# Optimization experiments

Measured on AMD Instinct MI355X. Metric: run time of the kernel, lower is better.

## Reference

```python
import jax, jax.numpy as jnp
import numpy as np

B, M, N, E = 64, 100, 6400, 102400   # graphs, nodes/graph, total nodes, edges
H, D, EMB, IMG, NC = 4, 512, 768, 1024, 2
HD = H * D
EPS = 1e-5


def _bn2(x, g, b, m, v):
    # BatchNorm1d eval mode on [B, C]
    return (x - m) / jnp.sqrt(v + EPS) * g + b


def _bn3(x, g, b, m, v):
    # BatchNorm1d eval mode on [B, C, L] -> channel dim is axis 1 (node index)
    return (x - m[None, :, None]) / jnp.sqrt(v + EPS)[None, :, None] * g[None, :, None] + b[None, :, None]


def _gat(feat, src, dst, W, al, ar, bias):
    # DGL GATConv (eval: feat_drop is identity). feat: [N, F_in]
    h = (feat @ W.T).reshape(-1, H, D)                 # [N, H, D]
    el = (h * al[None]).sum(-1)                         # [N, H]
    er = (h * ar[None]).sum(-1)                         # [N, H]
    e = jax.nn.leaky_relu(el[src] + er[dst], negative_slope=0.2)  # [E, H]
    mx = jax.ops.segment_max(e, dst, num_segments=N)
    a = jnp.exp(e - mx[dst])
    s = jax.ops.segment_sum(a, dst, num_segments=N)
    alpha = a / s[dst]                                  # edge softmax over incoming edges
    out = jax.ops.segment_sum(h[src] * alpha[:, :, None], dst, num_segments=N)  # [N, H, D]
    return out + bias.reshape(1, H, D)


def setup_inputs() -> dict:
    key = jax.random.key(0)
    ks = iter(jax.random.split(key, 80))
    n = lambda *s: jax.random.normal(next(ks), s, dtype=jnp.float32)

    def bn(c):
        return (1.0 + 0.1 * n(c), 0.1 * n(c), 0.1 * n(c),
                0.5 + jax.random.uniform(next(ks), (c,), dtype=jnp.float32))

    s = 0.02
    inp = {}
    inp['img_embedding'] = n(B, IMG)
    inp['func_text_embedding'] = n(B, EMB)
    inp['unix_emb'] = n(N, EMB)
    inp['pos_emb'] = jax.random.uniform(next(ks), (N, 4), dtype=jnp.float32)
    inp['src'] = jax.random.randint(next(ks), (E,), 0, N)
    inp['dst'] = jax.random.randint(next(ks), (E,), 0, N)
    inp['gat1_W'] = n(HD, EMB) * s; inp['gat1_al'] = n(H, D) * 0.1; inp['gat1_ar'] = n(H, D) * 0.1; inp['gat1_b'] = jnp.zeros(HD)
    inp['gat2_W'] = n(HD, HD) * s; inp['gat2_al'] = n(H, D) * 0.1; inp['gat2_ar'] = n(H, D) * 0.1; inp['gat2_b'] = jnp.zeros(HD)
    inp['fc_W'] = n(D, HD) * s; inp['fc_b'] = jnp.zeros(D)
    inp['hidden_W'] = n(8, D, D) * s; inp['hidden_b'] = jnp.zeros((8, D))
    inp['bn_text_g'], inp['bn_text_b'], inp['bn_text_m'], inp['bn_text_v'] = bn(EMB)
    inp['fc_text_W'] = n(D, EMB) * s; inp['fc_text_b'] = jnp.zeros(D)
    inp['swin_g'], inp['swin_b'], inp['swin_m'], inp['swin_v'] = bn(IMG)
    inp['swinfc_W'] = n(D, IMG) * s; inp['swinfc_b'] = jnp.zeros(D)
    inp['bngat_g'], inp['bngat_b'], inp['bngat_m'], inp['bngat_v'] = bn(M)
    inp['fc_gat_W'] = n(480, D) * s; inp['fc_gat_b'] = jnp.zeros(480)
    inp['bnbb_g'], inp['bnbb_b'], inp['bnbb_m'], inp['bnbb_v'] = bn(M)
    inp['fc_bbox_W'] = n(32, 4) * s; inp['fc_bbox_b'] = jnp.zeros(32)
    inp['fbn_g'], inp['fbn_b'], inp['fbn_m'], inp['fbn_v'] = bn(3 * D)
    inp['final_W'] = n(NC, 3 * D) * s; inp['final_b'] = jnp.zeros(NC)
    return inp


def reference(img_embedding, func_text_embedding, unix_emb, pos_emb, src, dst,
              gat1_W, gat1_al, gat1_ar, gat1_b, gat2_W, gat2_al, gat2_ar, gat2_b,
              fc_W, fc_b, hidden_W, hidden_b,
              bn_text_g, bn_text_b, bn_text_m, bn_text_v, fc_text_W, fc_text_b,
              swin_g, swin_b, swin_m, swin_v, swinfc_W, swinfc_b,
              bngat_g, bngat_b, bngat_m, bngat_v, fc_gat_W, fc_gat_b,
              bnbb_g, bnbb_b, bnbb_m, bnbb_v, fc_bbox_W, fc_bbox_b,
              fbn_g, fbn_b, fbn_m, fbn_v, final_W, final_b):
    # image branch
    x = jax.nn.elu(_bn2(img_embedding, swin_g, swin_b, swin_m, swin_v) @ swinfc_W.T + swinfc_b)
    # text branch
    ft = jax.nn.elu(_bn2(func_text_embedding, bn_text_g, bn_text_b, bn_text_m, bn_text_v) @ fc_text_W.T + fc_text_b)
    # graph branch: two stacked GATConv layers (dropout is identity in eval)
    h = _gat(unix_emb, src, dst, gat1_W, gat1_al, gat1_ar, gat1_b).reshape(N, HD)
    h = _gat(h, src, dst, gat2_W, gat2_al, gat2_ar, gat2_b).reshape(N, HD)
    h = jax.nn.elu(h @ fc_W.T + fc_b)
    for i in range(8):
        h = jax.nn.elu(h @ hidden_W[i].T + hidden_b[i])
    # unbatch + pad to max_node=100 -> pure reshape (all graphs have exactly M nodes)
    h_i = h.reshape(B, M, D)
    pos_i = pos_emb.reshape(B, M, 4)
    h_i = jax.nn.elu(_bn3(h_i, bngat_g, bngat_b, bngat_m, bngat_v) @ fc_gat_W.T + fc_gat_b)      # [B, M, 480]
    pos_i = jax.nn.elu(_bn3(pos_i, bnbb_g, bnbb_b, bnbb_m, bnbb_v) @ fc_bbox_W.T + fc_bbox_b)    # [B, M, 32]
    h_feature = jnp.concatenate([h_i, pos_i], axis=2).mean(axis=1)                                # [B, 512]
    all_feats = jnp.concatenate([x, h_feature, ft], axis=1)                                       # [B, 1536]
    return _bn2(all_feats, fbn_g, fbn_b, fbn_m, fbn_v) @ final_W.T + final_b
```

## Files before the change

### kernel.cpp

```cpp
#include <hip/hip_runtime.h>
#include <math.h>

#define Bg   64
#define Mg   100
#define Ng   6400
#define Eg   102400
#define Hh   4
#define Dd   512
#define HDd  2048
#define EMBd 768
#define IMGd 1024
#define EPSc 1e-5f

typedef __bf16 bf16x8 __attribute__((ext_vector_type(8)));
typedef float  f32x4  __attribute__((ext_vector_type(4)));

__device__ __forceinline__ float eluf(float x) { return x > 0.f ? x : expm1f(x); }

__device__ __forceinline__ unsigned short f2bf(float x) {
    unsigned int u = __builtin_bit_cast(unsigned int, x);
    u += 0x7FFFu + ((u >> 16) & 1u);
    return (unsigned short)(u >> 16);
}
__device__ __forceinline__ float bf2f(unsigned short s) {
    return __builtin_bit_cast(float, ((unsigned int)s) << 16);
}

__device__ __forceinline__ void gld16(const void* g, void* l) {
    __builtin_amdgcn_global_load_lds(
        (const __attribute__((address_space(1))) void*)g,
        (__attribute__((address_space(3))) void*)l, 16, 0, 0);
}

__global__ __launch_bounds__(256)
void gemm_bf16(const unsigned short* __restrict__ A,
               const unsigned short* __restrict__ W,
               const float* __restrict__ bias, void* __restrict__ C,
               int M, int N, int K, int act, int outbf)
{
    __shared__ __align__(16) unsigned short As[128 * 32];
    __shared__ __align__(16) unsigned short Bs[128 * 32];
    const int tid  = threadIdx.x;
    const int lane = tid & 63, wid = tid >> 6;
    const int bm = blockIdx.y * 128, bn = blockIdx.x * 128;
    const int wm = (wid >> 1) * 64, wn = (wid & 1) * 64;
    const int lrow = lane >> 2;
    const int lcol = (lane & 3) << 3;

    f32x4 acc[4][4] = {};

    const int ra = wid * 32;
    const unsigned short* gA0 = A + (size_t)(bm + ra + lrow) * K + lcol;
    const unsigned short* gA1 = A + (size_t)(bm + ra + 16 + lrow) * K + lcol;
    int rb0 = bn + ra + lrow;       if (rb0 >= N) rb0 = N - 1;
    int rb1 = bn + ra + 16 + lrow;  if (rb1 >= N) rb1 = N - 1;
    const unsigned short* gB0 = W + (size_t)rb0 * K + lcol;
    const unsigned short* gB1 = W + (size_t)rb1 * K + lcol;
    unsigned short* lA0 = &As[(ra)      * 32];
    unsigned short* lA1 = &As[(ra + 16) * 32];
    unsigned short* lB0 = &Bs[(ra)      * 32];
    unsigned short* lB1 = &Bs[(ra + 16) * 32];

    const int frow = lane & 15;
    const int quad = (lane >> 4) << 3;

    for (int k0 = 0; k0 < K; k0 += 32) {
        gld16(gA0 + k0, lA0);
        gld16(gA1 + k0, lA1);
        gld16(gB0 + k0, lB0);
        gld16(gB1 + k0, lB1);
        __syncthreads();
        bf16x8 af[4], bfr[4];
#pragma unroll
        for (int i = 0; i < 4; ++i)
            af[i]  = *(const bf16x8*)&As[(wm + i * 16 + frow) * 32 + quad];
#pragma unroll
        for (int i = 0; i < 4; ++i)
            bfr[i] = *(const bf16x8*)&Bs[(wn + i * 16 + frow) * 32 + quad];
#pragma unroll
        for (int mi = 0; mi < 4; ++mi)
#pragma unroll
            for (int ni = 0; ni < 4; ++ni)
                acc[mi][ni] = __builtin_amdgcn_mfma_f32_16x16x32_bf16(
                    af[mi], bfr[ni], acc[mi][ni], 0, 0, 0);
        __syncthreads();
    }

    const int crow0 = bm + wm + ((lane >> 4) << 2);
    const int ccol0 = bn + wn + (lane & 15);
#pragma unroll
    for (int mi = 0; mi < 4; ++mi) {
#pragma unroll
        for (int ni = 0; ni < 4; ++ni) {
            int col = ccol0 + ni * 16;
            if (col >= N) continue;
            float bv = bias ? bias[col] : 0.f;
#pragma unroll
            for (int r = 0; r < 4; ++r) {
                int row = crow0 + mi * 16 + r;
                float v = acc[mi][ni][r] + bv;
                if (act) v = eluf(v);
                if (outbf) ((unsigned short*)C)[(size_t)row * N + col] = f2bf(v);
                else       ((float*)C)[(size_t)row * N + col] = v;
            }
        }
    }
}

__global__ __launch_bounds__(256)
void gemm_bf16_t64(const unsigned short* __restrict__ A,
                   const unsigned short* __restrict__ W,
                   const float* __restrict__ bias, void* __restrict__ C,
                   int M, int N, int K, int act, int outbf)
{
    __shared__ __align__(16) unsigned short As[64 * 32];
    __shared__ __align__(16) unsigned short Bs[64 * 32];
    const int tid  = threadIdx.x;
    const int lane = tid & 63, wid = tid >> 6;
    const int bm = blockIdx.y * 64, bn = blockIdx.x * 64;
    const int wm = (wid >> 1) * 32, wn = (wid & 1) * 32;
    const int lrow = lane >> 2;
    const int lcol = (lane & 3) << 3;

    f32x4 acc[2][2] = {};

    const int ra = wid * 16;
    const unsigned short* gA = A + (size_t)(bm + ra + lrow) * K + lcol;
    int rb = bn + ra + lrow; if (rb >= N) rb = N - 1;
    const unsigned short* gB = W + (size_t)rb * K + lcol;
    unsigned short* lA = &As[ra * 32];
    unsigned short* lB = &Bs[ra * 32];

    const int frow = lane & 15;
    const int quad = (lane >> 4) << 3;

    for (int k0 = 0; k0 < K; k0 += 32) {
        gld16(gA + k0, lA);
        gld16(gB + k0, lB);
        __syncthreads();
        bf16x8 af0 = *(const bf16x8*)&As[(wm + frow) * 32 + quad];
        bf16x8 af1 = *(const bf16x8*)&As[(wm + 16 + frow) * 32 + quad];
        bf16x8 bf0 = *(const bf16x8*)&Bs[(wn + frow) * 32 + quad];
        bf16x8 bf1 = *(const bf16x8*)&Bs[(wn + 16 + frow) * 32 + quad];
        acc[0][0] = __builtin_amdgcn_mfma_f32_16x16x32_bf16(af0, bf0, acc[0][0], 0, 0, 0);
        acc[0][1] = __builtin_amdgcn_mfma_f32_16x16x32_bf16(af0, bf1, acc[0][1], 0, 0, 0);
        acc[1][0] = __builtin_amdgcn_mfma_f32_16x16x32_bf16(af1, bf0, acc[1][0], 0, 0, 0);
        acc[1][1] = __builtin_amdgcn_mfma_f32_16x16x32_bf16(af1, bf1, acc[1][1], 0, 0, 0);
        __syncthreads();
    }

    const int crow0 = bm + wm + ((lane >> 4) << 2);
    const int ccol0 = bn + wn + (lane & 15);
#pragma unroll
    for (int mi = 0; mi < 2; ++mi) {
#pragma unroll
        for (int ni = 0; ni < 2; ++ni) {
            int col = ccol0 + ni * 16;
            if (col >= N) continue;
            float bv = bias ? bias[col] : 0.f;
#pragma unroll
            for (int r = 0; r < 4; ++r) {
                int row = crow0 + mi * 16 + r;
                float v = acc[mi][ni][r] + bv;
                if (act) v = eluf(v);
                if (outbf) ((unsigned short*)C)[(size_t)row * N + col] = f2bf(v);
                else       ((float*)C)[(size_t)row * N + col] = v;
            }
        }
    }
}

__global__ __launch_bounds__(256)
void gemm_nt(const float* __restrict__ A, const float* __restrict__ W,
             const float* __restrict__ bias, float* __restrict__ C,
             int M, int N, int K, int act)
{
    __shared__ float As[16 * 68];
    __shared__ float Ws[16 * 68];
    const int tid = threadIdx.x;
    const int tx = tid & 15, ty = tid >> 4;
    const int bm = blockIdx.y * 64, bn = blockIdx.x * 64;
    const int lrow = tid >> 2;
    const int lk4  = (tid & 3) << 2;
    const int arow = bm + lrow;
    const int wrow = bn + lrow;
    const float* Aptr = A + (size_t)arow * K + lk4;
    const float* Wptr = W + (size_t)wrow * K + lk4;
    float acc[4][4] = {{0.f,0.f,0.f,0.f},{0.f,0.f,0.f,0.f},{0.f,0.f,0.f,0.f},{0.f,0.f,0.f,0.f}};

    for (int k0 = 0; k0 < K; k0 += 16) {
        float4 av = make_float4(0.f,0.f,0.f,0.f);
        float4 wv = make_float4(0.f,0.f,0.f,0.f);
        if (arow < M) av = *(const float4*)(Aptr + k0);
        if (wrow < N) wv = *(const float4*)(Wptr + k0);
        As[(lk4+0)*68 + lrow] = av.x;
        As[(lk4+1)*68 + lrow] = av.y;
        As[(lk4+2)*68 + lrow] = av.z;
        As[(lk4+3)*68 + lrow] = av.w;
        Ws[(lk4+0)*68 + lrow] = wv.x;
        Ws[(lk4+1)*68 + lrow] = wv.y;
        Ws[(lk4+2)*68 + lrow] = wv.z;
        Ws[(lk4+3)*68 + lrow] = wv.w;
        __syncthreads();
#pragma unroll
        for (int kk = 0; kk < 16; ++kk) {
            float4 a = *(const float4*)&As[kk*68 + (ty<<2)];
            float4 w = *(const float4*)&Ws[kk*68 + (tx<<2)];
            acc[0][0] += a.x*w.x; acc[0][1] += a.x*w.y; acc[0][2] += a.x*w.z; acc[0][3] += a.x*w.w;
            acc[1][0] += a.y*w.x; acc[1][1] += a.y*w.y; acc[1][2] += a.y*w.z; acc[1][3] += a.y*w.w;
            acc[2][0] += a.z*w.x; acc[2][1] += a.z*w.y; acc[2][2] += a.z*w.z; acc[2][3] += a.z*w.w;
            acc[3][0] += a.w*w.x; acc[3][1] += a.w*w.y; acc[3][2] += a.w*w.z; acc[3][3] += a.w*w.w;
        }
        __syncthreads();
    }

#pragma unroll
    for (int i = 0; i < 4; ++i) {
        int row = bm + (ty<<2) + i;
        int col = bn + (tx<<2);
        if (row < M && col < N) {
            float4 v;
            v.x = acc[i][0]; v.y = acc[i][1]; v.z = acc[i][2]; v.w = acc[i][3];
            if (bias) { v.x += bias[col]; v.y += bias[col+1]; v.z += bias[col+2]; v.w += bias[col+3]; }
            if (act == 1) { v.x = eluf(v.x); v.y = eluf(v.y); v.z = eluf(v.z); v.w = eluf(v.w); }
            *(float4*)(C + (size_t)row * N + col) = v;
        }
    }
}

struct CvtPack {
    const float* s[6];
    unsigned short* d[6];
    int n4[6];
};

__global__ void cvt_all(CvtPack p, int total4)
{
    int i = blockIdx.x * 256 + threadIdx.x;
    if (i >= total4) return;
#pragma unroll
    for (int k = 0; k < 6; ++k) {
        if (i < p.n4[k]) {
            float4 v = ((const float4*)p.s[k])[i];
            ushort4 o;
            o.x = f2bf(v.x); o.y = f2bf(v.y); o.z = f2bf(v.z); o.w = f2bf(v.w);
            ((ushort4*)p.d[k])[i] = o;
            return;
        }
        i -= p.n4[k];
    }
}

__global__ void bn_col(const float* __restrict__ x, const float* __restrict__ g,
                       const float* __restrict__ b, const float* __restrict__ m,
                       const float* __restrict__ v, float* __restrict__ y,
                       int rows, int cols)
{
    int i = blockIdx.x * 256 + threadIdx.x;
    if (i >= rows * cols) return;
    int c = i % cols;
    float inv = rsqrtf(v[c] + EPSc);
    y[i] = (x[i] - m[c]) * inv * g[c] + b[c];
}

__global__ void bn_node_b4(const ushort4* __restrict__ x, const float* __restrict__ g,
                           const float* __restrict__ b, const float* __restrict__ m,
                           const float* __restrict__ v, ushort4* __restrict__ y,
                           int total4, int Cdim4)
{
    int i = blockIdx.x * 256 + threadIdx.x;
    if (i >= total4) return;
    int n = i / Cdim4;
    int p = n % Mg;
    float sc = rsqrtf(v[p] + EPSc) * g[p];
    float sh = b[p] - m[p] * sc;
    ushort4 xv = x[i];
    ushort4 o;
    o.x = f2bf(bf2f(xv.x) * sc + sh);
    o.y = f2bf(bf2f(xv.y) * sc + sh);
    o.z = f2bf(bf2f(xv.z) * sc + sh);
    o.w = f2bf(bf2f(xv.w) * sc + sh);
    y[i] = o;
}

__global__ void zero_i32(int* __restrict__ p, int n)
{
    int i = blockIdx.x * 256 + threadIdx.x;
    if (i < n) p[i] = 0;
}

__global__ void count_dst(const int* __restrict__ dst, int* __restrict__ counts, int E)
{
    int i = blockIdx.x * 256 + threadIdx.x;
    if (i < E) atomicAdd(&counts[dst[i]], 1);
}

__global__ __launch_bounds__(1024)
void scan_excl(const int* __restrict__ counts, int* __restrict__ offs,
               int* __restrict__ cursor, int n)
{
    __shared__ int sm[1024];
    __shared__ int carry;
    if (threadIdx.x == 0) carry = 0;
    __syncthreads();
    for (int base = 0; base < n; base += 1024) {
        int i = base + (int)threadIdx.x;
        int v = (i < n) ? counts[i] : 0;
        sm[threadIdx.x] = v;
        __syncthreads();
        for (int o = 1; o < 1024; o <<= 1) {
            int t = (threadIdx.x >= (unsigned)o) ? sm[threadIdx.x - o] : 0;
            __syncthreads();
            sm[threadIdx.x] += t;
            __syncthreads();
        }
        int incl = sm[threadIdx.x];
        int myc = carry;
        if (i < n) {
            int ex = myc + incl - v;
            offs[i] = ex;
            cursor[i] = ex;
        }
        __syncthreads();
        if (threadIdx.x == 1023) carry = myc + sm[1023];
        __syncthreads();
    }
    if (threadIdx.x == 0) offs[n] = carry;
}

__global__ void scatter_edges(const int* __restrict__ dst, int* __restrict__ cursor,
                              int* __restrict__ eid, int E)
{
    int i = blockIdx.x * 256 + threadIdx.x;
    if (i < E) {
        int p = atomicAdd(&cursor[dst[i]], 1);
        eid[p] = i;
    }
}

__global__ __launch_bounds__(256)
void elr_kernel(const unsigned short* __restrict__ Hm, const float* __restrict__ al,
                const float* __restrict__ ar, float* __restrict__ el,
                float* __restrict__ er)
{
    int wid = threadIdx.x >> 6, lane = threadIdx.x & 63;
    int g = (blockIdx.x << 2) + wid;
    int n = g >> 2, h = g & 3;
    const unsigned short* hp = Hm + ((size_t)n << 11) + (h << 9) + (lane << 3);
    const float* alp = al + (h << 9) + (lane << 3);
    const float* arp = ar + (h << 9) + (lane << 3);
    ushort4 x0 = *(const ushort4*)hp;
    ushort4 x1 = *(const ushort4*)(hp + 4);
    float4 l0 = *(const float4*)alp, l1 = *(const float4*)(alp + 4);
    float4 r0 = *(const float4*)arp, r1 = *(const float4*)(arp + 4);
    float a0 = bf2f(x0.x), a1 = bf2f(x0.y), a2 = bf2f(x0.z), a3 = bf2f(x0.w);
    float a4 = bf2f(x1.x), a5 = bf2f(x1.y), a6 = bf2f(x1.z), a7 = bf2f(x1.w);
    float se = a0*l0.x + a1*l0.y + a2*l0.z + a3*l0.w + a4*l1.x + a5*l1.y + a6*l1.z + a7*l1.w;
    float sr = a0*r0.x + a1*r0.y + a2*r0.z + a3*r0.w + a4*r1.x + a5*r1.y + a6*r1.z + a7*r1.w;
#pragma unroll
    for (int o = 32; o > 0; o >>= 1) {
        se += __shfl_down(se, o, 64);
        sr += __shfl_down(sr, o, 64);
    }
    if (lane == 0) { el[g] = se; er[g] = sr; }
}

__global__ __launch_bounds__(256)
void gat_agg(const unsigned short* __restrict__ Hm, const float* __restrict__ el,
             const float* __restrict__ er, const int* __restrict__ src,
             const int* __restrict__ offs, const int* __restrict__ eid,
             const float* __restrict__ bias, unsigned short* __restrict__ out)
{
    int n = blockIdx.x;
    int tid = threadIdx.x;
    int beg = offs[n], end = offs[n + 1];
    int deg = end - beg;
    const int b0 = tid << 2;
    const int b1 = 1024 + (tid << 2);
    const int h0 = tid >> 7;
    const int h1 = h0 + 2;

    if (deg == 0) {
#pragma unroll
        for (int j = 0; j < 4; ++j) {
            out[((size_t)n << 11) + b0 + j] = f2bf(bias[b0 + j]);
            out[((size_t)n << 11) + b1 + j] = f2bf(bias[b1 + j]);
        }
        return;
    }

    __shared__ float m_sh[4], s_sh[4], al_sh[4];
    __shared__ int   src_sh[128];
    __shared__ float logit_sh[512];
    __shared__ float w_sh[512];

    if (tid < 4) { m_sh[tid] = -INFINITY; s_sh[tid] = 0.f; }
    float acc[8] = {0.f,0.f,0.f,0.f,0.f,0.f,0.f,0.f};
    __syncthreads();

    for (int c0 = 0; c0 < deg; c0 += 128) {
        int cnt = min(128, deg - c0);
        for (int i = tid; i < cnt; i += 256) src_sh[i] = src[eid[beg + c0 + i]];
        __syncthreads();
        for (int idx = tid; idx < (cnt << 2); idx += 256) {
            int i = idx >> 2, h = idx & 3;
            float x = el[(src_sh[i] << 2) + h] + er[(n << 2) + h];
            logit_sh[idx] = x > 0.f ? x : 0.2f * x;
        }
        __syncthreads();
        if (tid < 4) {
            float cm = -INFINITY;
            for (int i = 0; i < cnt; ++i) cm = fmaxf(cm, logit_sh[(i << 2) + tid]);
            float mn = fmaxf(m_sh[tid], cm);
            al_sh[tid] = expf(m_sh[tid] - mn);
            m_sh[tid] = mn;
        }
        __syncthreads();
        for (int idx = tid; idx < (cnt << 2); idx += 256)
            w_sh[idx] = expf(logit_sh[idx] - m_sh[idx & 3]);
        __syncthreads();
        if (tid < 4) {
            float cs = 0.f;
            for (int i = 0; i < cnt; ++i) cs += w_sh[(i << 2) + tid];
            s_sh[tid] = s_sh[tid] * al_sh[tid] + cs;
        }
        float r0 = al_sh[h0], r1 = al_sh[h1];
        acc[0] *= r0; acc[1] *= r0; acc[2] *= r0; acc[3] *= r0;
        acc[4] *= r1; acc[5] *= r1; acc[6] *= r1; acc[7] *= r1;
        for (int i = 0; i < cnt; ++i) {
            const unsigned short* hp = Hm + ((size_t)src_sh[i] << 11);
            ushort4 a = *(const ushort4*)(hp + b0);
            ushort4 b = *(const ushort4*)(hp + b1);
            float w0 = w_sh[(i << 2) + h0], w1 = w_sh[(i << 2) + h1];
            acc[0] += w0 * bf2f(a.x); acc[1] += w0 * bf2f(a.y);
            acc[2] += w0 * bf2f(a.z); acc[3] += w0 * bf2f(a.w);
            acc[4] += w1 * bf2f(b.x); acc[5] += w1 * bf2f(b.y);
            acc[6] += w1 * bf2f(b.z); acc[7] += w1 * bf2f(b.w);
        }
        __syncthreads();
    }

    float is0 = 1.f / s_sh[h0], is1 = 1.f / s_sh[h1];
#pragma unroll
    for (int j = 0; j < 4; ++j) {
        out[((size_t)n << 11) + b0 + j] = f2bf(acc[j] * is0 + bias[b0 + j]);
        out[((size_t)n << 11) + b1 + j] = f2bf(acc[4 + j] * is1 + bias[b1 + j]);
    }
}

__global__ void mean_kernel(const float* __restrict__ hg, const float* __restrict__ pos,
                            const float* __restrict__ bg, const float* __restrict__ bb_,
                            const float* __restrict__ bm_, const float* __restrict__ bv_,
                            const float* __restrict__ W, const float* __restrict__ bias,
                            float* __restrict__ hf)
{
    int i = blockIdx.x * 256 + threadIdx.x;
    if (i >= Bg * Dd) return;
    int bb = i >> 9, c = i & 511;
    float s = 0.f;
    if (c < 480) {
        const float* p = hg + (size_t)bb * Mg * 480 + c;
        for (int mm = 0; mm < Mg; ++mm) s += p[mm * 480];
    } else {
        int o = c - 480;
        float w0 = W[(o << 2) + 0], w1 = W[(o << 2) + 1];
        float w2 = W[(o << 2) + 2], w3 = W[(o << 2) + 3];
        float bo = bias[o];
        const float* pp = pos + (size_t)bb * Mg * 4;
        for (int mm = 0; mm < Mg; ++mm) {
            float sc = rsqrtf(bv_[mm] + EPSc) * bg[mm];
            float sh = bb_[mm] - bm_[mm] * sc;
            float a = bo + (pp[mm*4+0]*sc+sh)*w0 + (pp[mm*4+1]*sc+sh)*w1
                         + (pp[mm*4+2]*sc+sh)*w2 + (pp[mm*4+3]*sc+sh)*w3;
            s += eluf(a);
        }
    }
    hf[i] = s * 0.01f;
}

__global__ __launch_bounds__(256)
void final_kernel(const float* __restrict__ x, const float* __restrict__ hf,
                  const float* __restrict__ ft, const float* __restrict__ g,
                  const float* __restrict__ b, const float* __restrict__ m,
                  const float* __restrict__ v, const float* __restrict__ W,
                  const float* __restrict__ bias, float* __restrict__ out)
{
    int bb = blockIdx.x;
    int tid = threadIdx.x;
    float a0 = 0.f, a1 = 0.f;
    for (int c = tid; c < 1536; c += 256) {
        float xv = (c < 512) ? x[bb * 512 + c]
                 : (c < 1024) ? hf[bb * 512 + (c - 512)]
                              : ft[bb * 512 + (c - 1024)];
        float z = (xv - m[c]) * rsqrtf(v[c] + EPSc) * g[c] + b[c];
        a0 += z * W[c];
        a1 += z * W[1536 + c];
    }
    __shared__ float r0[256], r1[256];
    r0[tid] = a0; r1[tid] = a1;
    __syncthreads();
    for (int o = 128; o > 0; o >>= 1) {
        if (tid < o) { r0[tid] += r0[tid + o]; r1[tid] += r1[tid + o]; }
        __syncthreads();
    }
    if (tid == 0) {
        out[bb * 2 + 0] = r0[0] + bias[0];
        out[bb * 2 + 1] = r1[0] + bias[1];
    }
}

extern "C" void kernel_launch(void* const* d_in, const int* in_sizes, int n_in,
                              void* d_out, int out_size, void* d_ws, size_t ws_size,
                              hipStream_t stream)
{
    (void)in_sizes; (void)n_in; (void)out_size; (void)ws_size;

    const float* img   = (const float*)d_in[0];
    const float* ftxt  = (const float*)d_in[1];
    const float* unixe = (const float*)d_in[2];
    const float* pos   = (const float*)d_in[3];
    const int*   src   = (const int*)  d_in[4];
    const int*   dst   = (const int*)  d_in[5];
    const float* g1W   = (const float*)d_in[6];
    const float* g1al  = (const float*)d_in[7];
    const float* g1ar  = (const float*)d_in[8];
    const float* g1b   = (const float*)d_in[9];
    const float* g2W   = (const float*)d_in[10];
    const float* g2al  = (const float*)d_in[11];
    const float* g2ar  = (const float*)d_in[12];
    const float* g2b   = (const float*)d_in[13];
    const float* fcW   = (const float*)d_in[14];
    const float* fcb   = (const float*)d_in[15];
    const float* hidW  = (const float*)d_in[16];
    const float* hidb  = (const float*)d_in[17];
    const float* btg   = (const float*)d_in[18];
    const float* btb   = (const float*)d_in[19];
    const float* btm   = (const float*)d_in[20];
    const float* btv   = (const float*)d_in[21];
    const float* ftW   = (const float*)d_in[22];
    const float* ftbi  = (const float*)d_in[23];
    const float* swg   = (const float*)d_in[24];
    const float* swb   = (const float*)d_in[25];
    const float* swm   = (const float*)d_in[26];
    const float* swv   = (const float*)d_in[27];
    const float* swW   = (const float*)d_in[28];
    const float* swbi  = (const float*)d_in[29];
    const float* bgg   = (const float*)d_in[30];
    const float* bgb   = (const float*)d_in[31];
    const float* bgm   = (const float*)d_in[32];
    const float* bgv   = (const float*)d_in[33];
    const float* fgW   = (const float*)d_in[34];
    const float* fgb   = (const float*)d_in[35];
    const float* bbgp  = (const float*)d_in[36];
    const float* bbbp  = (const float*)d_in[37];
    const float* bbmp  = (const float*)d_in[38];
    const float* bbvp  = (const float*)d_in[39];
    const float* fbW   = (const float*)d_in[40];
    const float* fbb   = (const float*)d_in[41];
    const float* fng   = (const float*)d_in[42];
    const float* fnb   = (const float*)d_in[43];
    const float* fnm   = (const float*)d_in[44];
    const float* fnv   = (const float*)d_in[45];
    const float* fiW   = (const float*)d_in[46];
    const float* fib   = (const float*)d_in[47];
    float* out = (float*)d_out;

    char* p = (char*)d_ws;
    unsigned short* fA  = (unsigned short*)p; p += (size_t)Ng * HDd * 2;
    unsigned short* fB  = (unsigned short*)p; p += (size_t)Ng * HDd * 2;
    unsigned short* fC  = (unsigned short*)p; p += (size_t)Ng * Dd * 2;
    unsigned short* fD  = (unsigned short*)p; p += (size_t)Ng * Dd * 2;
    float*          fE  = (float*)p;          p += (size_t)Ng * 480 * 4;
    float*          el  = (float*)p;          p += (size_t)Ng * Hh * 4;
    float*          er  = (float*)p;          p += (size_t)Ng * Hh * 4;
    float*          xb  = (float*)p;          p += (size_t)Bg * Dd * 4;
    float*          ftb = (float*)p;          p += (size_t)Bg * Dd * 4;
    float*          hf  = (float*)p;          p += (size_t)Bg * Dd * 4;
    float*          ti  = (float*)p;          p += (size_t)Bg * IMGd * 4;
    float*          tt  = (float*)p;          p += (size_t)Bg * EMBd * 4;
    unsigned short* ubf = (unsigned short*)p; p += (size_t)Ng * EMBd * 2;
    unsigned short* wg1 = (unsigned short*)p; p += (size_t)HDd * EMBd * 2;
    unsigned short* wg2 = (unsigned short*)p; p += (size_t)HDd * HDd * 2;
    unsigned short* wfc = (unsigned short*)p; p += (size_t)Dd * HDd * 2;
    unsigned short* whid= (unsigned short*)p; p += (size_t)8 * Dd * Dd * 2;
    unsigned short* wfg = (unsigned short*)p; p += (size_t)480 * Dd * 2;
    int* counts = (int*)p; p += (size_t)Ng * 4;
    int* offs   = (int*)p; p += (size_t)(Ng + 1) * 4 + 12;
    int* cursor = (int*)p; p += (size_t)Ng * 4;
    int* eid    = (int*)p; p += (size_t)Eg * 4;

    CvtPack cp;
    cp.s[0] = unixe; cp.d[0] = ubf;  cp.n4[0] = Ng * EMBd / 4;
    cp.s[1] = g1W;   cp.d[1] = wg1;  cp.n4[1] = HDd * EMBd / 4;
    cp.s[2] = g2W;   cp.d[2] = wg2;  cp.n4[2] = HDd * HDd / 4;
    cp.s[3] = fcW;   cp.d[3] = wfc;  cp.n4[3] = Dd * HDd / 4;
    cp.s[4] = hidW;  cp.d[4] = whid; cp.n4[4] = 8 * Dd * Dd / 4;
    cp.s[5] = fgW;   cp.d[5] = wfg;  cp.n4[5] = 480 * Dd / 4;
    int total4 = cp.n4[0] + cp.n4[1] + cp.n4[2] + cp.n4[3] + cp.n4[4] + cp.n4[5];
    cvt_all<<<(total4 + 255)/256, 256, 0, stream>>>(cp, total4);

    bn_col<<<(Bg*IMGd + 255)/256, 256, 0, stream>>>(img, swg, swb, swm, swv, ti, Bg, IMGd);
    gemm_nt<<<dim3(8, 1), 256, 0, stream>>>(ti, swW, swbi, xb, Bg, Dd, IMGd, 1);
    bn_col<<<(Bg*EMBd + 255)/256, 256, 0, stream>>>(ftxt, btg, btb, btm, btv, tt, Bg, EMBd);
    gemm_nt<<<dim3(8, 1), 256, 0, stream>>>(tt, ftW, ftbi, ftb, Bg, Dd, EMBd, 1);

    zero_i32<<<(Ng + 255)/256, 256, 0, stream>>>(counts, Ng);
    count_dst<<<(Eg + 255)/256, 256, 0, stream>>>(dst, counts, Eg);
    scan_excl<<<1, 1024, 0, stream>>>(counts, offs, cursor, Ng);
    scatter_edges<<<(Eg + 255)/256, 256, 0, stream>>>(dst, cursor, eid, Eg);

    gemm_bf16<<<dim3(HDd/128, Ng/128), 256, 0, stream>>>(ubf, wg1, nullptr, fA, Ng, HDd, EMBd, 0, 1);
    elr_kernel<<<Ng, 256, 0, stream>>>(fA, g1al, g1ar, el, er);
    gat_agg<<<Ng, 256, 0, stream>>>(fA, el, er, src, offs, eid, g1b, fB);

    gemm_bf16<<<dim3(HDd/128, Ng/128), 256, 0, stream>>>(fB, wg2, nullptr, fA, Ng, HDd, HDd, 0, 1);
    elr_kernel<<<Ng, 256, 0, stream>>>(fA, g2al, g2ar, el, er);
    gat_agg<<<Ng, 256, 0, stream>>>(fA, el, er, src, offs, eid, g2b, fB);

    gemm_bf16_t64<<<dim3(Dd/64, Ng/64), 256, 0, stream>>>(fB, wfc, fcb, fC, Ng, Dd, HDd, 1, 1);

    unsigned short* cur = fC; unsigned short* nxt = fD;
    for (int i = 0; i < 8; ++i) {
        gemm_bf16_t64<<<dim3(Dd/64, Ng/64), 256, 0, stream>>>(
            cur, whid + (size_t)i * Dd * Dd, hidb + (size_t)i * Dd, nxt, Ng, Dd, Dd, 1, 1);
        unsigned short* t = cur; cur = nxt; nxt = t;
    }

    bn_node_b4<<<(Ng*Dd/4 + 255)/256, 256, 0, stream>>>(
        (const ushort4*)cur, bgg, bgb, bgm, bgv, (ushort4*)nxt, Ng*Dd/4, Dd/4);
    gemm_bf16_t64<<<dim3(8, Ng/64), 256, 0, stream>>>(nxt, wfg, fgb, fE, Ng, 480, Dd, 1, 0);

    mean_kernel<<<(Bg*Dd + 255)/256, 256, 0, stream>>>(fE, pos, bbgp, bbbp, bbmp, bbvp, fbW, fbb, hf);

    final_kernel<<<Bg, 256, 0, stream>>>(xb, hf, ftb, fng, fnb, fnm, fnv, fiW, fib, out);
}
```

Measured before the change: 845.1 us.

## Double-buffer LDS tiles in bf16 GEMM kernels to overlap loads with MFMA

Both bf16 MFMA GEMM kernels now use two LDS buffers for the A and B tiles. The global-to-LDS load for the next K-tile is issued before the current tile's fragment reads and MFMAs. This lets memory latency overlap with compute and removes one barrier per K step. In exchange, the shared memory per block doubles, which can lower occupancy.

```diff
diff --git a/kernel.cpp b/kernel.cpp
--- a/kernel.cpp
+++ b/kernel.cpp
@@ -38,8 +38,8 @@
                const float* __restrict__ bias, void* __restrict__ C,
                int M, int N, int K, int act, int outbf)
 {
-    __shared__ __align__(16) unsigned short As[128 * 32];
-    __shared__ __align__(16) unsigned short Bs[128 * 32];
+    __shared__ __align__(16) unsigned short As[2][128 * 32];
+    __shared__ __align__(16) unsigned short Bs[2][128 * 32];
     const int tid  = threadIdx.x;
     const int lane = tid & 63, wid = tid >> 6;
     const int bm = blockIdx.y * 128, bn = blockIdx.x * 128;
@@ -56,27 +56,34 @@
     int rb1 = bn + ra + 16 + lrow;  if (rb1 >= N) rb1 = N - 1;
     const unsigned short* gB0 = W + (size_t)rb0 * K + lcol;
     const unsigned short* gB1 = W + (size_t)rb1 * K + lcol;
-    unsigned short* lA0 = &As[(ra)      * 32];
-    unsigned short* lA1 = &As[(ra + 16) * 32];
-    unsigned short* lB0 = &Bs[(ra)      * 32];
-    unsigned short* lB1 = &Bs[(ra + 16) * 32];
 
     const int frow = lane & 15;
     const int quad = (lane >> 4) << 3;
-
-    for (int k0 = 0; k0 < K; k0 += 32) {
-        gld16(gA0 + k0, lA0);
-        gld16(gA1 + k0, lA1);
-        gld16(gB0 + k0, lB0);
-        gld16(gB1 + k0, lB1);
-        __syncthreads();
+    const int nt = K >> 5;
+
+    gld16(gA0, &As[0][ra * 32]);
+    gld16(gA1, &As[0][(ra + 16) * 32]);
+    gld16(gB0, &Bs[0][ra * 32]);
+    gld16(gB1, &Bs[0][(ra + 16) * 32]);
+    __syncthreads();
+
+    int cur = 0;
+    for (int t = 0; t < nt; ++t) {
+        if (t + 1 < nt) {
+            const int k0 = (t + 1) << 5;
+            const int nb = cur ^ 1;
+            gld16(gA0 + k0, &As[nb][ra * 32]);
+            gld16(gA1 + k0, &As[nb][(ra + 16) * 32]);
+            gld16(gB0 + k0, &Bs[nb][ra * 32]);
+            gld16(gB1 + k0, &Bs[nb][(ra + 16) * 32]);
+        }
         bf16x8 af[4], bfr[4];
 #pragma unroll
         for (int i = 0; i < 4; ++i)
-            af[i]  = *(const bf16x8*)&As[(wm + i * 16 + frow) * 32 + quad];
+            af[i]  = *(const bf16x8*)&As[cur][(wm + i * 16 + frow) * 32 + quad];
 #pragma unroll
         for (int i = 0; i < 4; ++i)
-            bfr[i] = *(const bf16x8*)&Bs[(wn + i * 16 + frow) * 32 + quad];
+            bfr[i] = *(const bf16x8*)&Bs[cur][(wn + i * 16 + frow) * 32 + quad];
 #pragma unroll
         for (int mi = 0; mi < 4; ++mi)
 #pragma unroll
@@ -84,6 +91,7 @@
                 acc[mi][ni] = __builtin_amdgcn_mfma_f32_16x16x32_bf16(
                     af[mi], bfr[ni], acc[mi][ni], 0, 0, 0);
         __syncthreads();
+        cur ^= 1;
     }
 
     const int crow0 = bm + wm + ((lane >> 4) << 2);
@@ -113,8 +121,8 @@
                    const float* __restrict__ bias, void* __restrict__ C,
                    int M, int N, int K, int act, int outbf)
 {
-    __shared__ __align__(16) unsigned short As[64 * 32];
-    __shared__ __align__(16) unsigned short Bs[64 * 32];
+    __shared__ __align__(16) unsigned short As[2][64 * 32];
+    __shared__ __align__(16) unsigned short Bs[2][64 * 32];
     const int tid  = threadIdx.x;
     const int lane = tid & 63, wid = tid >> 6;
     const int bm = blockIdx.y * 64, bn = blockIdx.x * 64;
@@ -128,25 +136,33 @@
     const unsigned short* gA = A + (size_t)(bm + ra + lrow) * K + lcol;
     int rb = bn + ra + lrow; if (rb >= N) rb = N - 1;
     const unsigned short* gB = W + (size_t)rb * K + lcol;
-    unsigned short* lA = &As[ra * 32];
-    unsigned short* lB = &Bs[ra * 32];
 
     const int frow = lane & 15;
     const int quad = (lane >> 4) << 3;
-
-    for (int k0 = 0; k0 < K; k0 += 32) {
-        gld16(gA + k0, lA);
-        gld16(gB + k0, lB);
-        __syncthreads();
-        bf16x8 af0 = *(const bf16x8*)&As[(wm + frow) * 32 + quad];
-        bf16x8 af1 = *(const bf16x8*)&As[(wm + 16 + frow) * 32 + quad];
-        bf16x8 bf0 = *(const bf16x8*)&Bs[(wn + frow) * 32 + quad];
-        bf16x8 bf1 = *(const bf16x8*)&Bs[(wn + 16 + frow) * 32 + quad];
+    const int nt = K >> 5;
+
+    gld16(gA, &As[0][ra * 32]);
+    gld16(gB, &Bs[0][ra * 32]);
+    __syncthreads();
+
+    int cur = 0;
+    for (int t = 0; t < nt; ++t) {
+        if (t + 1 < nt) {
+            const int k0 = (t + 1) << 5;
+            const int nb = cur ^ 1;
+            gld16(gA + k0, &As[nb][ra * 32]);
+            gld16(gB + k0, &Bs[nb][ra * 32]);
+        }
+        bf16x8 af0 = *(const bf16x8*)&As[cur][(wm + frow) * 32 + quad];
+        bf16x8 af1 = *(const bf16x8*)&As[cur][(wm + 16 + frow) * 32 + quad];
+        bf16x8 bf0 = *(const bf16x8*)&Bs[cur][(wn + frow) * 32 + quad];
+        bf16x8 bf1 = *(const bf16x8*)&Bs[cur][(wn + 16 + frow) * 32 + quad];
         acc[0][0] = __builtin_amdgcn_mfma_f32_16x16x32_bf16(af0, bf0, acc[0][0], 0, 0, 0);
         acc[0][1] = __builtin_amdgcn_mfma_f32_16x16x32_bf16(af0, bf1, acc[0][1], 0, 0, 0);
         acc[1][0] = __builtin_amdgcn_mfma_f32_16x16x32_bf16(af1, bf0, acc[1][0], 0, 0, 0);
         acc[1][1] = __builtin_amdgcn_mfma_f32_16x16x32_bf16(af1, bf1, acc[1][1], 0, 0, 0);
         __syncthreads();
+        cur ^= 1;
     }
 
     const int crow0 = bm + wm + ((lane >> 4) << 2);
```

After: 829.9 us. Within noise of the previous version (-1.8%).
